# Kernel optimization log

Measured on AMD Instinct MI355X. Metric: run time of the kernel, lower is better.

Reference implementation:

```python
import jax, jax.numpy as jnp
import numpy as np

NUM_VOCABS = 1024
OUTPUT_DIM = 1024  # enc_dim + dec_dim
ENC_DIM = 512
DEC_DIM = 512


def setup_inputs() -> dict:
    key = jax.random.key(0)
    k1, k2, k3, k4 = jax.random.split(key, 4)
    encoder_output = jax.random.normal(k1, (4, 256, ENC_DIM), dtype=jnp.float32)
    decoder_output = jax.random.normal(k2, (4, 64, DEC_DIM), dtype=jnp.float32)
    # nn.Linear(output_dim, num_vocabs): weight (V, output_dim), bias (V,)
    lim = 1.0 / np.sqrt(OUTPUT_DIM)
    W = jax.random.uniform(k3, (NUM_VOCABS, OUTPUT_DIM), dtype=jnp.float32, minval=-lim, maxval=lim)
    b = jax.random.uniform(k4, (NUM_VOCABS,), dtype=jnp.float32, minval=-lim, maxval=lim)
    return {"encoder_output": encoder_output, "decoder_output": decoder_output, "W": W, "b": b}


def reference(encoder_output, decoder_output, W, b):
    # Faithful to: cat(repeat(enc), repeat(dec)) @ W.T + b -> log_softmax
    # Equivalent efficient form: project enc and dec separately, broadcast-add.
    enc_dim = encoder_output.shape[-1]
    W_enc, W_dec = W[:, :enc_dim], W[:, enc_dim:]
    enc_proj = jnp.einsum('btd,vd->btv', encoder_output, W_enc)  # (B,T,V)
    dec_proj = jnp.einsum('bud,vd->buv', decoder_output, W_dec)  # (B,U,V)
    logits = enc_proj[:, :, None, :] + dec_proj[:, None, :, :] + b  # (B,T,U,V)
    return jax.nn.log_softmax(logits, axis=-1)
```

## Files before the change

### kernel.cpp

```cpp
#include <hip/hip_runtime.h>
#include <hip/hip_bf16.h>
#include <stdint.h>


#define KDIM 512
#define NV   1024
#define WDIM 1024

typedef __attribute__((ext_vector_type(8))) short short8;
typedef __attribute__((ext_vector_type(4))) float f32x4;

__device__ __forceinline__ ushort f2bf(float f) {
    uint32_t u = __float_as_uint(f);
    uint32_t r = (u + 0x7fffu + ((u >> 16) & 1u)) >> 16;
    return (ushort)r;
}

__global__ __launch_bounds__(256) void cvt_all(
        const float* __restrict__ enc, const float* __restrict__ dec,
        const float* __restrict__ W,
        ushort* __restrict__ encb, ushort* __restrict__ decb, ushort* __restrict__ wb) {
    int blk = blockIdx.x;
    const float* src; ushort* dst; int i;
    if (blk < 512)      { src = enc; dst = encb; i = blk * 256 + threadIdx.x; }
    else if (blk < 640) { src = dec; dst = decb; i = (blk - 512) * 256 + threadIdx.x; }
    else                { src = W;   dst = wb;   i = (blk - 640) * 256 + threadIdx.x; }
    f32x4 v = reinterpret_cast<const f32x4*>(src)[i];
    ushort4 h;
    h.x = f2bf(v.x); h.y = f2bf(v.y); h.z = f2bf(v.z); h.w = f2bf(v.w);
    reinterpret_cast<ushort4*>(dst)[i] = h;
}

__global__ __launch_bounds__(256) void gemm_proj(
        const ushort* __restrict__ encA, const ushort* __restrict__ decA,
        const ushort* __restrict__ Wb, const float* __restrict__ bias,
        float* __restrict__ encp, float* __restrict__ decp) {
    int tid = threadIdx.x;
    int lane = tid & 63, wid = tid >> 6;
    int wr = wid >> 1, wc = wid & 1;

    const ushort* A; float* out; int wcol_off, bm; bool use_bias;
    if (blockIdx.y < 16) { A = encA; out = encp; wcol_off = 0;   bm = blockIdx.y * 64;        use_bias = true;  }
    else                 { A = decA; out = decp; wcol_off = 512; bm = (blockIdx.y - 16) * 64; use_bias = false; }
    int bn = blockIdx.x * 64;
    int r16 = lane & 15, kg = lane >> 4;

    const ushort* a0p = A  + (size_t)(bm + wr * 32 + r16) * KDIM + kg * 8;
    const ushort* a1p = a0p + 16 * KDIM;
    const ushort* b0p = Wb + (size_t)(bn + wc * 32 + r16) * WDIM + wcol_off + kg * 8;
    const ushort* b1p = b0p + 16 * WDIM;

    f32x4 acc00 = {}, acc01 = {}, acc10 = {}, acc11 = {};
    #pragma unroll
    for (int ks = 0; ks < KDIM; ks += 32) {
        short8 a0 = *(const short8*)(a0p + ks);
        short8 a1 = *(const short8*)(a1p + ks);
        short8 b0 = *(const short8*)(b0p + ks);
        short8 b1 = *(const short8*)(b1p + ks);
        acc00 = __builtin_amdgcn_mfma_f32_16x16x32_bf16(a0, b0, acc00, 0, 0, 0);
        acc01 = __builtin_amdgcn_mfma_f32_16x16x32_bf16(a0, b1, acc01, 0, 0, 0);
        acc10 = __builtin_amdgcn_mfma_f32_16x16x32_bf16(a1, b0, acc10, 0, 0, 0);
        acc11 = __builtin_amdgcn_mfma_f32_16x16x32_bf16(a1, b1, acc11, 0, 0, 0);
    }

    int mb = bm + wr * 32 + (lane >> 4) * 4;
    int nb = bn + wc * 32 + (lane & 15);
    #pragma unroll
    for (int i = 0; i < 2; ++i) {
        #pragma unroll
        for (int j = 0; j < 2; ++j) {
            f32x4 acc = (i == 0) ? (j == 0 ? acc00 : acc01) : (j == 0 ? acc10 : acc11);
            int n = nb + j * 16;
            float bv = use_bias ? bias[n] : 0.0f;
            #pragma unroll
            for (int r = 0; r < 4; ++r) {
                int m = mb + i * 16 + r;
                out[(size_t)m * NV + n] = acc[r] + bv;
            }
        }
    }
}

__global__ __launch_bounds__(256) void lse_kernel(
        const float* __restrict__ encp, const float* __restrict__ decp,
        float* __restrict__ out) {
    int tid = threadIdx.x;
    int lane = tid & 63;
    int w = blockIdx.x * 4 + (tid >> 6);
    int bt = w >> 3;
    int ug = w & 7;
    int b = bt >> 8;

    const float* ep = encp + (size_t)bt * NV + lane * 4;
    f32x4 e0 = *(const f32x4*)(ep + 0);
    f32x4 e1 = *(const f32x4*)(ep + 256);
    f32x4 e2 = *(const f32x4*)(ep + 512);
    f32x4 e3 = *(const f32x4*)(ep + 768);

    const float* dbase = decp + (size_t)(b << 6) * NV + lane * 4;

    #pragma unroll
    for (int uu = 0; uu < 8; ++uu) {
        int u = ug * 8 + uu;
        const float* dp = dbase + (size_t)u * NV;
        f32x4 d0 = *(const f32x4*)(dp + 0)   + e0;
        f32x4 d1 = *(const f32x4*)(dp + 256) + e1;
        f32x4 d2 = *(const f32x4*)(dp + 512) + e2;
        f32x4 d3 = *(const f32x4*)(dp + 768) + e3;

        float s = __expf(d0.x) + __expf(d0.y) + __expf(d0.z) + __expf(d0.w)
                + __expf(d1.x) + __expf(d1.y) + __expf(d1.z) + __expf(d1.w)
                + __expf(d2.x) + __expf(d2.y) + __expf(d2.z) + __expf(d2.w)
                + __expf(d3.x) + __expf(d3.y) + __expf(d3.z) + __expf(d3.w);
        #pragma unroll
        for (int off = 32; off >= 1; off >>= 1)
            s += __shfl_xor(s, off, 64);
        float lse = __logf(s);

        float* op = out + (size_t)((bt << 6) | u) * NV + lane * 4;
        f32x4 lv = {lse, lse, lse, lse};
        *(f32x4*)(op + 0)   = d0 - lv;
        *(f32x4*)(op + 256) = d1 - lv;
        *(f32x4*)(op + 512) = d2 - lv;
        *(f32x4*)(op + 768) = d3 - lv;
    }
}

extern "C" void kernel_launch(void* const* d_in, const int* in_sizes, int n_in,
                              void* d_out, int out_size, void* d_ws, size_t ws_size,
                              hipStream_t stream) {
    const float* enc = (const float*)d_in[0];
    const float* dec = (const float*)d_in[1];
    const float* W   = (const float*)d_in[2];
    const float* b   = (const float*)d_in[3];
    float* out = (float*)d_out;

    char* ws = (char*)d_ws;
    float*  encp = (float*)(ws + 0);
    float*  decp = (float*)(ws + 4194304);
    ushort* encb = (ushort*)(ws + 5242880);
    ushort* decb = (ushort*)(ws + 6291456);
    ushort* wb   = (ushort*)(ws + 6553600);

    cvt_all<<<1664, 256, 0, stream>>>(enc, dec, W, encb, decb, wb);
    gemm_proj<<<dim3(16, 20), 256, 0, stream>>>(encb, decb, wb, b, encp, decp);
    lse_kernel<<<2048, 256, 0, stream>>>(encp, decp, out);
}
```

Before: 71.75 us.

## Stage decoder projection rows in LDS and share across eight waves

The LSE kernel now uses 512-thread blocks where eight waves, each handling a different encoder time step, share one group of eight decoder rows loaded once into shared memory. Before, each wave read its decoder rows straight from global memory, so the same rows were fetched by many waves. The output is 256MB-scale writes, so the kernel is likely bound by store bandwidth. The extra reuse may matter little, and the 32KB LDS allocation plus a barrier could lower occupancy.

```diff
diff --git a/kernel.cpp b/kernel.cpp
--- a/kernel.cpp
+++ b/kernel.cpp
@@ -81,15 +81,25 @@
     }
 }
 
-__global__ __launch_bounds__(256) void lse_kernel(
+__global__ __launch_bounds__(512) void lse_kernel(
         const float* __restrict__ encp, const float* __restrict__ decp,
         float* __restrict__ out) {
-    int tid = threadIdx.x;
+    int tid  = threadIdx.x;
     int lane = tid & 63;
-    int w = blockIdx.x * 4 + (tid >> 6);
-    int bt = w >> 3;
-    int ug = w & 7;
-    int b = bt >> 8;
+    int wv   = tid >> 6;
+    int blk  = blockIdx.x;
+    int b    = blk >> 8;
+    int tg   = (blk >> 3) & 31;
+    int ug   = blk & 7;
+    int bt   = (b << 8) | (tg * 8 + wv);
+
+    __shared__ float dls[8 * NV];
+
+    const f32x4* dsrc = (const f32x4*)(decp + (size_t)((b << 6) | (ug * 8)) * NV);
+    f32x4* ddst = (f32x4*)dls;
+    #pragma unroll
+    for (int i = 0; i < 4; ++i)
+        ddst[tid + i * 512] = dsrc[tid + i * 512];
 
     const float* ep = encp + (size_t)bt * NV + lane * 4;
     f32x4 e0 = *(const f32x4*)(ep + 0);
@@ -97,16 +107,17 @@
     f32x4 e2 = *(const f32x4*)(ep + 512);
     f32x4 e3 = *(const f32x4*)(ep + 768);
 
-    const float* dbase = decp + (size_t)(b << 6) * NV + lane * 4;
+    __syncthreads();
+
+    float* obase = out + ((size_t)(bt << 6) + ug * 8) * NV + lane * 4;
 
     #pragma unroll
     for (int uu = 0; uu < 8; ++uu) {
-        int u = ug * 8 + uu;
-        const float* dp = dbase + (size_t)u * NV;
-        f32x4 d0 = *(const f32x4*)(dp + 0)   + e0;
-        f32x4 d1 = *(const f32x4*)(dp + 256) + e1;
-        f32x4 d2 = *(const f32x4*)(dp + 512) + e2;
-        f32x4 d3 = *(const f32x4*)(dp + 768) + e3;
+        const float* dl = dls + uu * NV + lane * 4;
+        f32x4 d0 = *(const f32x4*)(dl + 0)   + e0;
+        f32x4 d1 = *(const f32x4*)(dl + 256) + e1;
+        f32x4 d2 = *(const f32x4*)(dl + 512) + e2;
+        f32x4 d3 = *(const f32x4*)(dl + 768) + e3;
 
         float s = __expf(d0.x) + __expf(d0.y) + __expf(d0.z) + __expf(d0.w)
                 + __expf(d1.x) + __expf(d1.y) + __expf(d1.z) + __expf(d1.w)
@@ -117,7 +128,7 @@
             s += __shfl_xor(s, off, 64);
         float lse = __logf(s);
 
-        float* op = out + (size_t)((bt << 6) | u) * NV + lane * 4;
+        float* op = obase + (size_t)uu * NV;
         f32x4 lv = {lse, lse, lse, lse};
         *(f32x4*)(op + 0)   = d0 - lv;
         *(f32x4*)(op + 256) = d1 - lv;
@@ -144,5 +155,5 @@
 
     cvt_all<<<1664, 256, 0, stream>>>(enc, dec, W, encb, decb, wb);
     gemm_proj<<<dim3(16, 20), 256, 0, stream>>>(encb, decb, wb, b, encp, decp);
-    lse_kernel<<<2048, 256, 0, stream>>>(encp, decp, out);
+    lse_kernel<<<1024, 512, 0, stream>>>(encp, decp, out);
 }
```

Result: slower. 73.86 us (+2.9%).
